# Kernel tuning notes

Measured on AMD Instinct MI355X. Metric: run time of the kernel, lower is better.

## Reference

```python
import jax, jax.numpy as jnp
import numpy as np

B, T, N_OBS, H, N_ACT = 128, 512, 256, 512, 32


def setup_inputs() -> dict:
    key = jax.random.key(0)
    ks = jax.random.split(key, 9)
    s = lambda fan_in: 1.0 / np.sqrt(fan_in)
    return {
        "obs_seq": jax.random.normal(ks[0], (B, T, N_OBS), jnp.float32),
        "h0": jax.random.normal(ks[1], (B, H), jnp.float32),
        "c0": jax.random.normal(ks[2], (B, H), jnp.float32),
        "Wx": jax.random.normal(ks[3], (N_OBS, 4 * H), jnp.float32) * s(N_OBS),
        "Wh": jax.random.normal(ks[4], (H, 4 * H), jnp.float32) * s(H),
        "b": jnp.zeros((4 * H,), jnp.float32),
        "W1": jax.random.normal(ks[5], (H, 512), jnp.float32) * s(H),
        "b1": jnp.zeros((512,), jnp.float32),
        "W2": jax.random.normal(ks[6], (512, 512), jnp.float32) * s(512),
        "b2": jnp.zeros((512,), jnp.float32),
        "Wo": jax.random.normal(ks[7], (512, N_ACT), jnp.float32) * s(512),
        "bo": jnp.zeros((N_ACT,), jnp.float32),
        "action_min": jnp.zeros((N_ACT,), jnp.float32),
        "action_max": jnp.ones((N_ACT,), jnp.float32),
    }


def reference(obs_seq, h0, c0, Wx, Wh, b, W1, b1, W2, b2, Wo, bo, action_min, action_max):
    # Pre-compute input-to-gate projections for all timesteps in one big GEMM,
    # matching flax LSTMCell math: dense_i (no bias) on x, dense_h (bias) on h.
    xg = jnp.einsum('btf,fg->btg', obs_seq, Wx)  # (B, T, 4H)

    def step(carry, xg_t):
        h, c = carry
        z = xg_t + h @ Wh + b  # (B, 4H)
        i, f, g, o = jnp.split(z, 4, axis=-1)
        c = jax.nn.sigmoid(f) * c + jax.nn.sigmoid(i) * jnp.tanh(g)
        h = jax.nn.sigmoid(o) * jnp.tanh(c)
        return (h, c), h

    (h_T, c_T), ys = jax.lax.scan(step, (h0, c0), jnp.swapaxes(xg, 0, 1))
    x = jnp.swapaxes(ys, 0, 1)  # (B, T, H)

    x = jax.nn.relu(x @ W1 + b1)
    x = jax.nn.relu(x @ W2 + b2)
    x = jnp.tanh(x @ Wo + bo)
    action = 0.5 * (x * (action_max - action_min) + (action_max + action_min))
    return action, h_T, c_T
```

## Files before the change

kernel.cpp:

```cpp
#include <hip/hip_runtime.h>

typedef unsigned short u16;
typedef unsigned int u32;
typedef unsigned long long ull;
typedef __attribute__((ext_vector_type(8))) short bf16x8;
typedef __attribute__((ext_vector_type(4))) float f32x4;
typedef __attribute__((ext_vector_type(4))) unsigned u32x4;

#define B_   128
#define T_   512
#define NOBS 256
#define H_   512
#define G4   2048
#define NACT 32
#define M_   (B_*T_)
#define GR   8
#define ROWS 16
#define UN   16
#define ZW   66
#define SENT 0x7FC07FC0u

__device__ __forceinline__ float b2f(u16 s) {
  union { unsigned u; float f; } v; v.u = ((unsigned)s) << 16; return v.f;
}
__device__ __forceinline__ u16 f2b(float f) {
  union { float f; unsigned u; } v; v.f = f;
  unsigned r = v.u + 0x7FFFu + ((v.u >> 16) & 1u);
  return (u16)(r >> 16);
}
__device__ __forceinline__ float sigm(float x) { return 1.f/(1.f+__expf(-x)); }
__device__ __forceinline__ float tanh_f(float x) { return 1.f - 2.f/(1.f+__expf(2.f*x)); }

__device__ __forceinline__ void gld16(const void* g, void* ldsbase) {
#if __has_builtin(__builtin_amdgcn_global_load_lds)
  __builtin_amdgcn_global_load_lds((const __attribute__((address_space(1))) void*)g,
                                   (__attribute__((address_space(3))) void*)ldsbase, 16, 0, 0);
#else
  ((float4*)ldsbase)[threadIdx.x & 63] = *(const float4*)g;
#endif
}

__global__ void k_cvt_obsT(const float* __restrict__ in, u16* __restrict__ out) {
  const long i = (long)blockIdx.x*blockDim.x + threadIdx.x;
  const int k8 = (int)(i & (NOBS/8 - 1));
  const long row = i >> 5;
  const int t = (int)(row >> 7), b = (int)(row & (B_-1));
  const float* src = in + ((long)b*T_ + t)*NOBS + k8*8;
  ushort2 o[4];
  #pragma unroll
  for (int q = 0; q < 4; ++q) {
    o[q].x = f2b(src[q*2]);
    o[q].y = f2b(src[q*2+1]);
  }
  *(ushort2*)&out[i*8+0] = o[0]; *(ushort2*)&out[i*8+2] = o[1];
  *(ushort2*)&out[i*8+4] = o[2]; *(ushort2*)&out[i*8+6] = o[3];
}

__global__ void k_inith(const float* __restrict__ h0, u16* __restrict__ hp) {
  const int i = blockIdx.x*256 + threadIdx.x;
  const int plane = i >> 15, off = i & 32767;
  u32 v;
  if (plane == 0) {
    const int row = off >> 8, p = off & 255;
    v = (unsigned)f2b(h0[row*H_ + 2*p]) | ((unsigned)f2b(h0[row*H_ + 2*p + 1]) << 16);
  } else {
    v = SENT;
  }
  ((u32*)hp)[i] = v;
}

__global__ void k_prep_wT(const float* __restrict__ Wx, const float* __restrict__ Wh,
                          const float* __restrict__ W1, const float* __restrict__ W2,
                          const float* __restrict__ Wo,
                          u16* __restrict__ WxT, u16* __restrict__ WhT,
                          u16* __restrict__ W1T, u16* __restrict__ W2T,
                          u16* __restrict__ WoT) {
  int i = blockIdx.x*256 + threadIdx.x;
  const float* in; u16* out; int R, C;
  if (i < 524288)        { in = Wx; out = WxT; R = NOBS; C = G4; }
  else if (i < 1572864)  { i -= 524288;  in = Wh; out = WhT; R = H_; C = G4; }
  else if (i < 1835008)  { i -= 1572864; in = W1; out = W1T; R = H_; C = H_; }
  else if (i < 2097152)  { i -= 1835008; in = W2; out = W2T; R = H_; C = H_; }
  else                   { i -= 2097152; in = Wo; out = WoT; R = H_; C = NACT; }
  const int c = i / R, r = i - c*R;
  out[i] = f2b(in[r*C + c]);
}

template<int EPI>
__global__ __launch_bounds__(256) void k_gemm_bt(const u16* __restrict__ A, const u16* __restrict__ BT,
                                                 u16* __restrict__ C, const float* __restrict__ bias,
                                                 int M, int N, int K)
{
  __shared__ u16 As[128*64];
  __shared__ u16 Bs[128*64];
  const int tid = threadIdx.x, wv = tid >> 6, lane = tid & 63;
  const int ntile = N >> 7;
  const int tm = blockIdx.x / ntile, tn = blockIdx.x - tm*ntile;
  const int wr = wv >> 1, wc = wv & 1;
  f32x4 acc[4][4];
  for (int m=0;m<4;++m) for (int n=0;n<4;++n) acc[m][n] = (f32x4){0.f,0.f,0.f,0.f};
  const long abase = (long)tm*128, bbase = (long)tn*128;
  const int kit = K >> 6;
  for (int kt = 0; kt < kit; ++kt) {
    const int k0 = kt << 6;
    #pragma unroll
    for (int q = 0; q < 4; ++q) {
      int off = (wv*4+q)*1024 + lane*16;
      int row = off >> 7, colb = off & 127;
      gld16((const char*)A  + ((abase+row)*K + k0)*2 + colb, (char*)As + (wv*4+q)*1024);
      gld16((const char*)BT + ((bbase+row)*K + k0)*2 + colb, (char*)Bs + (wv*4+q)*1024);
    }
    asm volatile("s_waitcnt vmcnt(0)" ::: "memory");
    __syncthreads();
    const int kg = (lane >> 4) * 8;
    #pragma unroll
    for (int kk = 0; kk < 64; kk += 32) {
      bf16x8 af[4], bfr[4];
      #pragma unroll
      for (int m = 0; m < 4; ++m)
        af[m] = *(const bf16x8*)(As + (wr*64 + m*16 + (lane&15))*64 + kk + kg);
      #pragma unroll
      for (int n = 0; n < 4; ++n)
        bfr[n] = *(const bf16x8*)(Bs + (wc*64 + n*16 + (lane&15))*64 + kk + kg);
      #pragma unroll
      for (int m = 0; m < 4; ++m)
        #pragma unroll
        for (int n = 0; n < 4; ++n)
          acc[m][n] = __builtin_amdgcn_mfma_f32_16x16x32_bf16(af[m], bfr[n], acc[m][n], 0, 0, 0);
    }
    __syncthreads();
  }
  const int rq = (lane >> 4) * 4, cl = lane & 15;
  #pragma unroll
  for (int n = 0; n < 4; ++n) {
    const int coln = (int)bbase + wc*64 + n*16 + cl;
    const float bv = (EPI == 1) ? bias[coln] : 0.f;
    #pragma unroll
    for (int m = 0; m < 4; ++m) {
      const long rowb = abase + wr*64 + m*16 + rq;
      #pragma unroll
      for (int q = 0; q < 4; ++q) {
        float v = acc[m][n][q];
        if (EPI == 1) v = fmaxf(v + bv, 0.f);
        C[(rowb+q)*(long)N + coln] = f2b(v);
      }
    }
  }
}

__global__ __launch_bounds__(256, 1) void k_scan(
    const u16* __restrict__ obsT, const u16* __restrict__ WxT, const u16* __restrict__ WhT,
    const float* __restrict__ bvec, const float* __restrict__ c0f,
    u16* __restrict__ hp,
    u16* __restrict__ ys, float* __restrict__ outh, float* __restrict__ outc)
{
  __shared__ u16 Bw[96*64*8];
  __shared__ float zs[2][16*ZW];
  __shared__ float cst[256];
  __shared__ float bsl[64];

  const int tid = threadIdx.x, wv = tid >> 6, lane = tid & 63;
  const int wg = blockIdx.x, isl = wg & (GR-1), cg = wg >> 3;
  const int rb0 = isl*ROWS, S0 = cg*UN;

  const int kh = wv >> 1, ch = wv & 1;
  const int C0 = ch*32;
  const int lq = lane >> 4, l15 = lane & 15;
  const int arow = rb0 + l15;

  for (int idx = tid; idx < 96*64; idx += 256) {
    const int kg = idx >> 6, col = idx & 63;
    const long jrow = (long)((col >> 4)*H_ + S0 + (col & 15));
    const u16* src = (kg < 32) ? (WxT + jrow*NOBS + kg*8)
                               : (WhT + jrow*H_ + (long)(kg-32)*8);
    *(bf16x8*)(Bw + (long)idx*8) = *(const bf16x8*)src;
  }
  cst[tid] = c0f[(rb0 + (tid >> 4))*H_ + S0 + (tid & 15)];
  if (tid < 64) bsl[tid] = bvec[(tid >> 4)*H_ + S0 + (tid & 15)];
  __syncthreads();

  const long fofs = (long)arow*H_ + kh*256 + lq*8;
  const int ldsC = (C0 + l15)*8;

  bf16x8 ax[4];
  {
    const u16* Ax = obsT + (long)arow*NOBS + kh*128 + lq*8;
    #pragma unroll
    for (int ks = 0; ks < 4; ++ks) ax[ks] = *(const bf16x8*)(Ax + ks*32);
  }

  for (int t = 0; t < T_; ++t) {
    f32x4 acc0 = {0.f,0.f,0.f,0.f}, acc1 = {0.f,0.f,0.f,0.f};
    union { u32x4 u; bf16x8 v; } hf[8];
    const u16* haddr = hp + ((long)(t & 7) << 16) + fofs;

    asm volatile("s_waitcnt vmcnt(0)" ::: "memory");

    #pragma unroll
    for (int ks = 0; ks < 8; ++ks)
      asm volatile("global_load_dwordx4 %0, %1, off offset:%2 sc0 sc1"
                   : "=v"(hf[ks].u) : "v"(haddr), "i"(ks*64));

    #pragma unroll
    for (int ks = 0; ks < 4; ++ks) {
      const u16* bp = Bw + (kh*16 + ks*4 + lq)*512 + ldsC;
      bf16x8 b0 = *(const bf16x8*)bp;
      bf16x8 b1 = *(const bf16x8*)(bp + 128);
      acc0 = __builtin_amdgcn_mfma_f32_16x16x32_bf16(ax[ks], b0, acc0, 0, 0, 0);
      acc1 = __builtin_amdgcn_mfma_f32_16x16x32_bf16(ax[ks], b1, acc1, 0, 0, 0);
    }
    __builtin_amdgcn_sched_barrier(0);

    {
      asm volatile("s_waitcnt vmcnt(0)" ::: "memory");
      __builtin_amdgcn_sched_barrier(0);
      unsigned ready = 1u;
      #pragma unroll
      for (int ks = 0; ks < 8; ++ks)
        #pragma unroll
        for (int j = 0; j < 4; ++j)
          ready &= (hf[ks].u[j] != SENT) ? 1u : 0u;
      if (!__all((int)ready)) {
        int spin = 1 << 12;
        for (;;) {
          #pragma unroll
          for (int ks = 0; ks < 8; ++ks)
            asm volatile("global_load_dwordx4 %0, %1, off offset:%2 sc0 sc1"
                         : "=v"(hf[ks].u) : "v"(haddr), "i"(ks*64));
          asm volatile("s_waitcnt vmcnt(0)" ::: "memory");
          __builtin_amdgcn_sched_barrier(0);
          unsigned rdy = 1u;
          #pragma unroll
          for (int ks = 0; ks < 8; ++ks)
            #pragma unroll
            for (int j = 0; j < 4; ++j)
              rdy &= (hf[ks].u[j] != SENT) ? 1u : 0u;
          if (__all((int)rdy)) break;
          if (--spin == 0) break;
        }
      }
    }

    bf16x8 axn[4];
    {
      const int tn = (t+1 < T_) ? t+1 : t;
      const u16* Axn = obsT + ((long)tn*B_ + arow)*NOBS + kh*128 + lq*8;
      #pragma unroll
      for (int ks = 0; ks < 4; ++ks) axn[ks] = *(const bf16x8*)(Axn + ks*32);
    }

    #pragma unroll
    for (int ks = 0; ks < 8; ++ks) {
      const u16* bp = Bw + (32 + kh*32 + ks*4 + lq)*512 + ldsC;
      bf16x8 b0 = *(const bf16x8*)bp;
      bf16x8 b1 = *(const bf16x8*)(bp + 128);
      acc0 = __builtin_amdgcn_mfma_f32_16x16x32_bf16(hf[ks].v, b0, acc0, 0, 0, 0);
      acc1 = __builtin_amdgcn_mfma_f32_16x16x32_bf16(hf[ks].v, b1, acc1, 0, 0, 0);
    }
    #pragma unroll
    for (int ks = 0; ks < 4; ++ks) ax[ks] = axn[ks];

    {
      const int zr0 = lq*4, zc = C0 + l15;
      #pragma unroll
      for (int q = 0; q < 4; ++q) {
        zs[kh][(zr0+q)*ZW + zc]      = acc0[q];
        zs[kh][(zr0+q)*ZW + zc + 16] = acc1[q];
      }
    }
    __syncthreads();

    if (tid < 128) {
      const int rr = tid >> 3, pp = tid & 7;
      float hv2[2], cn2[2];
      #pragma unroll
      for (int u = 0; u < 2; ++u) {
        const int sl = 2*pp + u;
        const float* z0 = &zs[0][rr*ZW];
        const float* z1 = &zs[1][rr*ZW];
        const float zi = z0[sl]    + z1[sl]    + bsl[sl];
        const float zf = z0[16+sl] + z1[16+sl] + bsl[16+sl];
        const float zg = z0[32+sl] + z1[32+sl] + bsl[32+sl];
        const float zo = z0[48+sl] + z1[48+sl] + bsl[48+sl];
        const float cv = cst[rr*16 + sl];
        const float cn = sigm(zf)*cv + sigm(zi)*tanh_f(zg);
        hv2[u] = sigm(zo)*tanh_f(cn);
        cn2[u] = cn;
        cst[rr*16 + sl] = cn;
      }
      const unsigned h01 = (unsigned)f2b(hv2[0]) | ((unsigned)f2b(hv2[1]) << 16);
      const int bq = rb0 + rr;
      const long wofs = (long)bq*H_ + S0 + 2*pp;
      if (t < T_-1)
        __hip_atomic_store((u32*)(hp + ((long)((t+1) & 7) << 16) + wofs), h01,
                           __ATOMIC_RELAXED, __HIP_MEMORY_SCOPE_AGENT);
      __hip_atomic_store((u32*)(hp + ((long)((t+5) & 7) << 16) + wofs), SENT,
                         __ATOMIC_RELAXED, __HIP_MEMORY_SCOPE_AGENT);
      *(u32*)(ys + ((long)bq*T_ + t)*H_ + S0 + 2*pp) = h01;
      if (t == T_-1) {
        outh[bq*H_ + S0 + 2*pp]     = hv2[0];
        outh[bq*H_ + S0 + 2*pp + 1] = hv2[1];
        outc[bq*H_ + S0 + 2*pp]     = cn2[0];
        outc[bq*H_ + S0 + 2*pp + 1] = cn2[1];
      }
    }
  }
}

#define WSW 520
__global__ __launch_bounds__(256) void k_head_mfma(const u16* __restrict__ X,
    const u16* __restrict__ WoT, const float* __restrict__ bo,
    const float* __restrict__ amin, const float* __restrict__ amax,
    float* __restrict__ out)
{
  __shared__ u16 Ws[NACT*WSW];
  const int tid = threadIdx.x, wv = tid >> 6, lane = tid & 63;
  #pragma unroll
  for (int q = 0; q < 8; ++q) {
    const int chunk = q*256 + tid, r = chunk >> 6, c = chunk & 63;
    *(float4*)(Ws + r*WSW + c*8) = ((const float4*)WoT)[chunk];
  }
  __syncthreads();
  const int lq = lane >> 4, l15 = lane & 15;
  const long rb = (long)blockIdx.x*64 + wv*16;
  const u16* Ab = X + (rb + l15)*H_ + lq*8;
  f32x4 acc0 = {0.f,0.f,0.f,0.f}, acc1 = {0.f,0.f,0.f,0.f};
  #pragma unroll
  for (int ks = 0; ks < 16; ++ks) {
    bf16x8 a  = *(const bf16x8*)(Ab + ks*32);
    bf16x8 b0 = *(const bf16x8*)(Ws + l15*WSW + ks*32 + lq*8);
    bf16x8 b1 = *(const bf16x8*)(Ws + (16+l15)*WSW + ks*32 + lq*8);
    acc0 = __builtin_amdgcn_mfma_f32_16x16x32_bf16(a, b0, acc0, 0, 0, 0);
    acc1 = __builtin_amdgcn_mfma_f32_16x16x32_bf16(a, b1, acc1, 0, 0, 0);
  }
  const int c0 = l15, c1 = 16 + l15;
  const float bo0 = bo[c0], bo1 = bo[c1];
  const float a0 = amin[c0], A0 = amax[c0], a1 = amin[c1], A1 = amax[c1];
  #pragma unroll
  for (int q = 0; q < 4; ++q) {
    const long r = rb + lq*4 + q;
    const float y0 = tanh_f(acc0[q] + bo0), y1 = tanh_f(acc1[q] + bo1);
    out[r*NACT + c0] = 0.5f*(y0*(A0 - a0) + (A0 + a0));
    out[r*NACT + c1] = 0.5f*(y1*(A1 - a1) + (A1 + a1));
  }
}

extern "C" void kernel_launch(void* const* d_in, const int* in_sizes, int n_in,
                              void* d_out, int out_size, void* d_ws, size_t ws_size,
                              hipStream_t stream) {
  const float* obs = (const float*)d_in[0];
  const float* h0  = (const float*)d_in[1];
  const float* c0  = (const float*)d_in[2];
  const float* Wx  = (const float*)d_in[3];
  const float* Wh  = (const float*)d_in[4];
  const float* bb  = (const float*)d_in[5];
  const float* W1  = (const float*)d_in[6];
  const float* b1  = (const float*)d_in[7];
  const float* W2  = (const float*)d_in[8];
  const float* b2  = (const float*)d_in[9];
  const float* Wo  = (const float*)d_in[10];
  const float* bo  = (const float*)d_in[11];
  const float* amin= (const float*)d_in[12];
  const float* amax= (const float*)d_in[13];

  char* ws = (char*)d_ws;
  u16* obsT  = (u16*)(ws + 0);
  u16* ys    = (u16*)(ws + 33554432);
  u16* t1    = (u16*)(ws + 100663296);
  u16* t2    = (u16*)(ws + 33554432);
  u16* hp    = (u16*)(ws + 100663296);
  u16* WxT   = (u16*)(ws + 167772160);
  u16* WhT   = (u16*)(ws + 168820736);
  u16* W1T   = (u16*)(ws + 170917888);
  u16* W2T   = (u16*)(ws + 171442176);
  u16* WoT   = (u16*)(ws + 171966464);

  float* outA = (float*)d_out;
  float* outh = outA + (long)M_*NACT;
  float* outc = outh + B_*H_;

  k_cvt_obsT<<<M_*NOBS/8/256, 256, 0, stream>>>(obs, obsT);
  k_inith<<<1024, 256, 0, stream>>>(h0, hp);
  k_prep_wT<<<8256, 256, 0, stream>>>(Wx, Wh, W1, W2, Wo, WxT, WhT, W1T, W2T, WoT);

  k_scan<<<256, 256, 0, stream>>>(obsT, WxT, WhT, bb, c0, hp, ys, outh, outc);

  k_gemm_bt<1><<<(M_/128)*(H_/128), 256, 0, stream>>>(ys, W1T, t1, b1, M_, H_, H_);
  k_gemm_bt<1><<<(M_/128)*(H_/128), 256, 0, stream>>>(t1, W2T, t2, b2, M_, H_, H_);
  k_head_mfma<<<M_/64, 256, 0, stream>>>(t2, WoT, bo, amin, amax, outA);
}
```

Measured before the change: 1.473 ms.

## Keep scan weights in registers and pack two column slices per block

The persistent LSTM scan kernel now holds each wave's Wx and Wh weight fragments in VGPRs for all timesteps instead of reading them from LDS every step. It also merges two column-slice workgroups into one 512-thread block, so the grid is 128 blocks of 512 threads instead of 256 of 256, with per-slice shared buffers for gate partial sums, cell state and bias. This removes per-step LDS weight traffic from the serial recurrence. The cost is much higher register pressure (24 bf16x8 weight vectors per lane) with possible spills, and a block-wide barrier that now couples two slices.

After: 2.756 ms. +87.0%, slower.

```diff
diff --git a/kernel.cpp b/kernel.cpp
--- a/kernel.cpp
+++ b/kernel.cpp
@@ -148,39 +148,52 @@
   }
 }
 
-__global__ __launch_bounds__(256, 1) void k_scan(
+__global__ __launch_bounds__(512, 1) void k_scan(
     const u16* __restrict__ obsT, const u16* __restrict__ WxT, const u16* __restrict__ WhT,
     const float* __restrict__ bvec, const float* __restrict__ c0f,
     u16* __restrict__ hp,
     u16* __restrict__ ys, float* __restrict__ outh, float* __restrict__ outc)
 {
-  __shared__ u16 Bw[96*64*8];
-  __shared__ float zs[2][16*ZW];
-  __shared__ float cst[256];
-  __shared__ float bsl[64];
-
-  const int tid = threadIdx.x, wv = tid >> 6, lane = tid & 63;
-  const int wg = blockIdx.x, isl = wg & (GR-1), cg = wg >> 3;
+  __shared__ float zs[2][2][16*ZW];
+  __shared__ float cst[2][256];
+  __shared__ float bsl[2][64];
+
+  const int tid = threadIdx.x;
+  const int slice = tid >> 8;
+  const int ltid = tid & 255;
+  const int wv4 = (tid >> 6) & 3;
+  const int lane = tid & 63;
+  const int wg = blockIdx.x, isl = wg & (GR-1), sgrp = wg >> 3;
+  const int cg = sgrp*2 + slice;
   const int rb0 = isl*ROWS, S0 = cg*UN;
 
-  const int kh = wv >> 1, ch = wv & 1;
+  const int kh = wv4 >> 1, ch = wv4 & 1;
   const int C0 = ch*32;
   const int lq = lane >> 4, l15 = lane & 15;
   const int arow = rb0 + l15;
 
-  for (int idx = tid; idx < 96*64; idx += 256) {
-    const int kg = idx >> 6, col = idx & 63;
-    const long jrow = (long)((col >> 4)*H_ + S0 + (col & 15));
-    const u16* src = (kg < 32) ? (WxT + jrow*NOBS + kg*8)
-                               : (WhT + jrow*H_ + (long)(kg-32)*8);
-    *(bf16x8*)(Bw + (long)idx*8) = *(const bf16x8*)src;
-  }
-  cst[tid] = c0f[(rb0 + (tid >> 4))*H_ + S0 + (tid & 15)];
-  if (tid < 64) bsl[tid] = bvec[(tid >> 4)*H_ + S0 + (tid & 15)];
+  const int j0 = C0 + l15, j1 = j0 + 16;
+  const long w0 = (long)((j0 >> 4)*H_ + S0 + (j0 & 15));
+  const long w1 = (long)((j1 >> 4)*H_ + S0 + (j1 & 15));
+  bf16x8 wbx[4][2], wbh[8][2];
+  #pragma unroll
+  for (int ks = 0; ks < 4; ++ks) {
+    const long k = (long)kh*128 + ks*32 + lq*8;
+    wbx[ks][0] = *(const bf16x8*)(WxT + w0*NOBS + k);
+    wbx[ks][1] = *(const bf16x8*)(WxT + w1*NOBS + k);
+  }
+  #pragma unroll
+  for (int ks = 0; ks < 8; ++ks) {
+    const long k = (long)kh*256 + ks*32 + lq*8;
+    wbh[ks][0] = *(const bf16x8*)(WhT + w0*H_ + k);
+    wbh[ks][1] = *(const bf16x8*)(WhT + w1*H_ + k);
+  }
+
+  cst[slice][ltid] = c0f[(rb0 + (ltid >> 4))*H_ + S0 + (ltid & 15)];
+  if (ltid < 64) bsl[slice][ltid] = bvec[(ltid >> 4)*H_ + S0 + (ltid & 15)];
   __syncthreads();
 
   const long fofs = (long)arow*H_ + kh*256 + lq*8;
-  const int ldsC = (C0 + l15)*8;
 
   bf16x8 ax[4];
   {
@@ -203,11 +216,8 @@
 
     #pragma unroll
     for (int ks = 0; ks < 4; ++ks) {
-      const u16* bp = Bw + (kh*16 + ks*4 + lq)*512 + ldsC;
-      bf16x8 b0 = *(const bf16x8*)bp;
-      bf16x8 b1 = *(const bf16x8*)(bp + 128);
-      acc0 = __builtin_amdgcn_mfma_f32_16x16x32_bf16(ax[ks], b0, acc0, 0, 0, 0);
-      acc1 = __builtin_amdgcn_mfma_f32_16x16x32_bf16(ax[ks], b1, acc1, 0, 0, 0);
+      acc0 = __builtin_amdgcn_mfma_f32_16x16x32_bf16(ax[ks], wbx[ks][0], acc0, 0, 0, 0);
+      acc1 = __builtin_amdgcn_mfma_f32_16x16x32_bf16(ax[ks], wbx[ks][1], acc1, 0, 0, 0);
     }
     __builtin_amdgcn_sched_barrier(0);
 
@@ -251,11 +261,8 @@
 
     #pragma unroll
     for (int ks = 0; ks < 8; ++ks) {
-      const u16* bp = Bw + (32 + kh*32 + ks*4 + lq)*512 + ldsC;
-      bf16x8 b0 = *(const bf16x8*)bp;
-      bf16x8 b1 = *(const bf16x8*)(bp + 128);
-      acc0 = __builtin_amdgcn_mfma_f32_16x16x32_bf16(hf[ks].v, b0, acc0, 0, 0, 0);
-      acc1 = __builtin_amdgcn_mfma_f32_16x16x32_bf16(hf[ks].v, b1, acc1, 0, 0, 0);
+      acc0 = __builtin_amdgcn_mfma_f32_16x16x32_bf16(hf[ks].v, wbh[ks][0], acc0, 0, 0, 0);
+      acc1 = __builtin_amdgcn_mfma_f32_16x16x32_bf16(hf[ks].v, wbh[ks][1], acc1, 0, 0, 0);
     }
     #pragma unroll
     for (int ks = 0; ks < 4; ++ks) ax[ks] = axn[ks];
@@ -264,29 +271,29 @@
       const int zr0 = lq*4, zc = C0 + l15;
       #pragma unroll
       for (int q = 0; q < 4; ++q) {
-        zs[kh][(zr0+q)*ZW + zc]      = acc0[q];
-        zs[kh][(zr0+q)*ZW + zc + 16] = acc1[q];
+        zs[slice][kh][(zr0+q)*ZW + zc]      = acc0[q];
+        zs[slice][kh][(zr0+q)*ZW + zc + 16] = acc1[q];
       }
     }
     __syncthreads();
 
-    if (tid < 128) {
-      const int rr = tid >> 3, pp = tid & 7;
+    if (ltid < 128) {
+      const int rr = ltid >> 3, pp = ltid & 7;
       float hv2[2], cn2[2];
       #pragma unroll
       for (int u = 0; u < 2; ++u) {
         const int sl = 2*pp + u;
-        const float* z0 = &zs[0][rr*ZW];
-        const float* z1 = &zs[1][rr*ZW];
-        const float zi = z0[sl]    + z1[sl]    + bsl[sl];
-        const float zf = z0[16+sl] + z1[16+sl] + bsl[16+sl];
-        const float zg = z0[32+sl] + z1[32+sl] + bsl[32+sl];
-        const float zo = z0[48+sl] + z1[48+sl] + bsl[48+sl];
-        const float cv = cst[rr*16 + sl];
+        const float* z0 = &zs[slice][0][rr*ZW];
+        const float* z1 = &zs[slice][1][rr*ZW];
+        const float zi = z0[sl]    + z1[sl]    + bsl[slice][sl];
+        const float zf = z0[16+sl] + z1[16+sl] + bsl[slice][16+sl];
+        const float zg = z0[32+sl] + z1[32+sl] + bsl[slice][32+sl];
+        const float zo = z0[48+sl] + z1[48+sl] + bsl[slice][48+sl];
+        const float cv = cst[slice][rr*16 + sl];
         const float cn = sigm(zf)*cv + sigm(zi)*tanh_f(zg);
         hv2[u] = sigm(zo)*tanh_f(cn);
         cn2[u] = cn;
-        cst[rr*16 + sl] = cn;
+        cst[slice][rr*16 + sl] = cn;
       }
       const unsigned h01 = (unsigned)f2b(hv2[0]) | ((unsigned)f2b(hv2[1]) << 16);
       const int bq = rb0 + rr;
@@ -383,7 +390,7 @@
   k_inith<<<1024, 256, 0, stream>>>(h0, hp);
   k_prep_wT<<<8256, 256, 0, stream>>>(Wx, Wh, W1, W2, Wo, WxT, WhT, W1T, W2T, WoT);
 
-  k_scan<<<256, 256, 0, stream>>>(obsT, WxT, WhT, bb, c0, hp, ys, outh, outc);
+  k_scan<<<128, 512, 0, stream>>>(obsT, WxT, WhT, bb, c0, hp, ys, outh, outc);
 
   k_gemm_bt<1><<<(M_/128)*(H_/128), 256, 0, stream>>>(ys, W1T, t1, b1, M_, H_, H_);
   k_gemm_bt<1><<<(M_/128)*(H_/128), 256, 0, stream>>>(t1, W2T, t2, b2, M_, H_, H_);
```

## Interleave four batch sub-groups per workgroup in the LSTM scan

Applied to the files above, without the earlier changes.

Each scan workgroup now owns four interleaved 4-row batch sub-groups instead of one contiguous 16-row slab. Each timestep processes the sub-groups in turn: it loads h, spin-waits for readiness, runs the MFMA, applies the gates, and publishes the new h. The intent is that while one sub-group waits on other workgroups' h, another sub-group's data is likely already ready, which hides the cross-workgroup synchronisation latency. The cost is more serial rounds and barriers per step. The MFMA also computes 16 rows where only 4 are distinct, and only 32 threads do the gate math.

After: 4.077 ms. 177% more time.

```diff
diff --git a/kernel.cpp b/kernel.cpp
--- a/kernel.cpp
+++ b/kernel.cpp
@@ -14,8 +14,7 @@
 #define G4   2048
 #define NACT 32
 #define M_   (B_*T_)
-#define GR   8
-#define ROWS 16
+#define NS   4
 #define UN   16
 #define ZW   66
 #define SENT 0x7FC07FC0u
@@ -155,18 +154,18 @@
     u16* __restrict__ ys, float* __restrict__ outh, float* __restrict__ outc)
 {
   __shared__ u16 Bw[96*64*8];
-  __shared__ float zs[2][16*ZW];
-  __shared__ float cst[256];
+  __shared__ float zs[2][2][16*ZW];
+  __shared__ float cst[NS][64];
   __shared__ float bsl[64];
 
   const int tid = threadIdx.x, wv = tid >> 6, lane = tid & 63;
-  const int wg = blockIdx.x, isl = wg & (GR-1), cg = wg >> 3;
-  const int rb0 = isl*ROWS, S0 = cg*UN;
+  const int wg = blockIdx.x, g = wg & 7, cg = wg >> 3;
+  const int S0 = cg*UN;
 
   const int kh = wv >> 1, ch = wv & 1;
   const int C0 = ch*32;
   const int lq = lane >> 4, l15 = lane & 15;
-  const int arow = rb0 + l15;
+  const int r4 = l15 & 3;
 
   for (int idx = tid; idx < 96*64; idx += 256) {
     const int kg = idx >> 6, col = idx & 63;
@@ -175,133 +174,141 @@
                                : (WhT + jrow*H_ + (long)(kg-32)*8);
     *(bf16x8*)(Bw + (long)idx*8) = *(const bf16x8*)src;
   }
-  cst[tid] = c0f[(rb0 + (tid >> 4))*H_ + S0 + (tid & 15)];
-  if (tid < 64) bsl[tid] = bvec[(tid >> 4)*H_ + S0 + (tid & 15)];
+  if (tid < 64) {
+    bsl[tid] = bvec[(tid >> 4)*H_ + S0 + (tid & 15)];
+    #pragma unroll
+    for (int s = 0; s < NS; ++s)
+      cst[s][tid] = c0f[(4*g + 32*s + (tid >> 4))*H_ + S0 + (tid & 15)];
+  }
   __syncthreads();
 
-  const long fofs = (long)arow*H_ + kh*256 + lq*8;
   const int ldsC = (C0 + l15)*8;
 
-  bf16x8 ax[4];
-  {
+  bf16x8 ax[NS][4];
+  #pragma unroll
+  for (int s = 0; s < NS; ++s) {
+    const int arow = 4*g + 32*s + r4;
     const u16* Ax = obsT + (long)arow*NOBS + kh*128 + lq*8;
     #pragma unroll
-    for (int ks = 0; ks < 4; ++ks) ax[ks] = *(const bf16x8*)(Ax + ks*32);
+    for (int ks = 0; ks < 4; ++ks) ax[s][ks] = *(const bf16x8*)(Ax + ks*32);
   }
 
   for (int t = 0; t < T_; ++t) {
-    f32x4 acc0 = {0.f,0.f,0.f,0.f}, acc1 = {0.f,0.f,0.f,0.f};
-    union { u32x4 u; bf16x8 v; } hf[8];
-    const u16* haddr = hp + ((long)(t & 7) << 16) + fofs;
-
-    asm volatile("s_waitcnt vmcnt(0)" ::: "memory");
-
-    #pragma unroll
-    for (int ks = 0; ks < 8; ++ks)
-      asm volatile("global_load_dwordx4 %0, %1, off offset:%2 sc0 sc1"
-                   : "=v"(hf[ks].u) : "v"(haddr), "i"(ks*64));
-
-    #pragma unroll
-    for (int ks = 0; ks < 4; ++ks) {
-      const u16* bp = Bw + (kh*16 + ks*4 + lq)*512 + ldsC;
-      bf16x8 b0 = *(const bf16x8*)bp;
-      bf16x8 b1 = *(const bf16x8*)(bp + 128);
-      acc0 = __builtin_amdgcn_mfma_f32_16x16x32_bf16(ax[ks], b0, acc0, 0, 0, 0);
-      acc1 = __builtin_amdgcn_mfma_f32_16x16x32_bf16(ax[ks], b1, acc1, 0, 0, 0);
-    }
-    __builtin_amdgcn_sched_barrier(0);
-
-    {
+    #pragma unroll
+    for (int s = 0; s < NS; ++s) {
+      const int rb0 = 4*g + 32*s;
+      const int arow = rb0 + r4;
+      const long fofs = (long)arow*H_ + kh*256 + lq*8;
+      const u16* haddr = hp + ((long)(t & 7) << 16) + fofs;
+
       asm volatile("s_waitcnt vmcnt(0)" ::: "memory");
+
+      union { u32x4 u; bf16x8 v; } hf[8];
+      #pragma unroll
+      for (int ks = 0; ks < 8; ++ks)
+        asm volatile("global_load_dwordx4 %0, %1, off offset:%2 sc0 sc1"
+                     : "=v"(hf[ks].u) : "v"(haddr), "i"(ks*64));
+
+      f32x4 acc0 = {0.f,0.f,0.f,0.f}, acc1 = {0.f,0.f,0.f,0.f};
+      #pragma unroll
+      for (int ks = 0; ks < 4; ++ks) {
+        const u16* bp = Bw + (kh*16 + ks*4 + lq)*512 + ldsC;
+        bf16x8 b0 = *(const bf16x8*)bp;
+        bf16x8 b1 = *(const bf16x8*)(bp + 128);
+        acc0 = __builtin_amdgcn_mfma_f32_16x16x32_bf16(ax[s][ks], b0, acc0, 0, 0, 0);
+        acc1 = __builtin_amdgcn_mfma_f32_16x16x32_bf16(ax[s][ks], b1, acc1, 0, 0, 0);
+      }
       __builtin_amdgcn_sched_barrier(0);
-      unsigned ready = 1u;
-      #pragma unroll
-      for (int ks = 0; ks < 8; ++ks)
-        #pragma unroll
-        for (int j = 0; j < 4; ++j)
-          ready &= (hf[ks].u[j] != SENT) ? 1u : 0u;
-      if (!__all((int)ready)) {
-        int spin = 1 << 12;
-        for (;;) {
+
+      {
+        asm volatile("s_waitcnt vmcnt(0)" ::: "memory");
+        __builtin_amdgcn_sched_barrier(0);
+        unsigned ready = 1u;
+        #pragma unroll
+        for (int ks = 0; ks < 8; ++ks)
           #pragma unroll
-          for (int ks = 0; ks < 8; ++ks)
-            asm volatile("global_load_dwordx4 %0, %1, off offset:%2 sc0 sc1"
-                         : "=v"(hf[ks].u) : "v"(haddr), "i"(ks*64));
-          asm volatile("s_waitcnt vmcnt(0)" ::: "memory");
-          __builtin_amdgcn_sched_barrier(0);
-          unsigned rdy = 1u;
-          #pragma unroll
-          for (int ks = 0; ks < 8; ++ks)
+          for (int j = 0; j < 4; ++j)
+            ready &= (hf[ks].u[j] != SENT) ? 1u : 0u;
+        if (!__all((int)ready)) {
+          int spin = 1 << 12;
+          for (;;) {
             #pragma unroll
-            for (int j = 0; j < 4; ++j)
-              rdy &= (hf[ks].u[j] != SENT) ? 1u : 0u;
-          if (__all((int)rdy)) break;
-          if (--spin == 0) break;
+            for (int ks = 0; ks < 8; ++ks)
+              asm volatile("global_load_dwordx4 %0, %1, off offset:%2 sc0 sc1"
+                           : "=v"(hf[ks].u) : "v"(haddr), "i"(ks*64));
+            asm volatile("s_waitcnt vmcnt(0)" ::: "memory");
+            __builtin_amdgcn_sched_barrier(0);
+            unsigned rdy = 1u;
+            #pragma unroll
+            for (int ks = 0; ks < 8; ++ks)
+              #pragma unroll
+              for (int j = 0; j < 4; ++j)
+                rdy &= (hf[ks].u[j] != SENT) ? 1u : 0u;
+            if (__all((int)rdy)) break;
+            if (--spin == 0) break;
+          }
         }
       }
-    }
-
-    bf16x8 axn[4];
-    {
-      const int tn = (t+1 < T_) ? t+1 : t;
-      const u16* Axn = obsT + ((long)tn*B_ + arow)*NOBS + kh*128 + lq*8;
-      #pragma unroll
-      for (int ks = 0; ks < 4; ++ks) axn[ks] = *(const bf16x8*)(Axn + ks*32);
-    }
-
-    #pragma unroll
-    for (int ks = 0; ks < 8; ++ks) {
-      const u16* bp = Bw + (32 + kh*32 + ks*4 + lq)*512 + ldsC;
-      bf16x8 b0 = *(const bf16x8*)bp;
-      bf16x8 b1 = *(const bf16x8*)(bp + 128);
-      acc0 = __builtin_amdgcn_mfma_f32_16x16x32_bf16(hf[ks].v, b0, acc0, 0, 0, 0);
-      acc1 = __builtin_amdgcn_mfma_f32_16x16x32_bf16(hf[ks].v, b1, acc1, 0, 0, 0);
-    }
-    #pragma unroll
-    for (int ks = 0; ks < 4; ++ks) ax[ks] = axn[ks];
-
-    {
-      const int zr0 = lq*4, zc = C0 + l15;
-      #pragma unroll
-      for (int q = 0; q < 4; ++q) {
-        zs[kh][(zr0+q)*ZW + zc]      = acc0[q];
-        zs[kh][(zr0+q)*ZW + zc + 16] = acc1[q];
-      }
-    }
-    __syncthreads();
-
-    if (tid < 128) {
-      const int rr = tid >> 3, pp = tid & 7;
-      float hv2[2], cn2[2];
-      #pragma unroll
-      for (int u = 0; u < 2; ++u) {
-        const int sl = 2*pp + u;
-        const float* z0 = &zs[0][rr*ZW];
-        const float* z1 = &zs[1][rr*ZW];
-        const float zi = z0[sl]    + z1[sl]    + bsl[sl];
-        const float zf = z0[16+sl] + z1[16+sl] + bsl[16+sl];
-        const float zg = z0[32+sl] + z1[32+sl] + bsl[32+sl];
-        const float zo = z0[48+sl] + z1[48+sl] + bsl[48+sl];
-        const float cv = cst[rr*16 + sl];
-        const float cn = sigm(zf)*cv + sigm(zi)*tanh_f(zg);
-        hv2[u] = sigm(zo)*tanh_f(cn);
-        cn2[u] = cn;
-        cst[rr*16 + sl] = cn;
-      }
-      const unsigned h01 = (unsigned)f2b(hv2[0]) | ((unsigned)f2b(hv2[1]) << 16);
-      const int bq = rb0 + rr;
-      const long wofs = (long)bq*H_ + S0 + 2*pp;
-      if (t < T_-1)
-        __hip_atomic_store((u32*)(hp + ((long)((t+1) & 7) << 16) + wofs), h01,
+
+      {
+        const int tn = (t+1 < T_) ? t+1 : t;
+        const u16* Axn = obsT + ((long)tn*B_ + arow)*NOBS + kh*128 + lq*8;
+        #pragma unroll
+        for (int ks = 0; ks < 4; ++ks) ax[s][ks] = *(const bf16x8*)(Axn + ks*32);
+      }
+
+      #pragma unroll
+      for (int ks = 0; ks < 8; ++ks) {
+        const u16* bp = Bw + (32 + kh*32 + ks*4 + lq)*512 + ldsC;
+        bf16x8 b0 = *(const bf16x8*)bp;
+        bf16x8 b1 = *(const bf16x8*)(bp + 128);
+        acc0 = __builtin_amdgcn_mfma_f32_16x16x32_bf16(hf[ks].v, b0, acc0, 0, 0, 0);
+        acc1 = __builtin_amdgcn_mfma_f32_16x16x32_bf16(hf[ks].v, b1, acc1, 0, 0, 0);
+      }
+
+      {
+        const int zr0 = lq*4, zc = C0 + l15;
+        #pragma unroll
+        for (int q = 0; q < 4; ++q) {
+          zs[s & 1][kh][(zr0+q)*ZW + zc]      = acc0[q];
+          zs[s & 1][kh][(zr0+q)*ZW + zc + 16] = acc1[q];
+        }
+      }
+      __syncthreads();
+
+      if (tid < 32) {
+        const int rr = tid >> 3, pp = tid & 7;
+        float hv2[2], cn2[2];
+        #pragma unroll
+        for (int u = 0; u < 2; ++u) {
+          const int sl = 2*pp + u;
+          const float* z0 = &zs[s & 1][0][rr*ZW];
+          const float* z1 = &zs[s & 1][1][rr*ZW];
+          const float zi = z0[sl]    + z1[sl]    + bsl[sl];
+          const float zf = z0[16+sl] + z1[16+sl] + bsl[16+sl];
+          const float zg = z0[32+sl] + z1[32+sl] + bsl[32+sl];
+          const float zo = z0[48+sl] + z1[48+sl] + bsl[48+sl];
+          const float cv = cst[s][rr*16 + sl];
+          const float cn = sigm(zf)*cv + sigm(zi)*tanh_f(zg);
+          hv2[u] = sigm(zo)*tanh_f(cn);
+          cn2[u] = cn;
+          cst[s][rr*16 + sl] = cn;
+        }
+        const unsigned h01 = (unsigned)f2b(hv2[0]) | ((unsigned)f2b(hv2[1]) << 16);
+        const int bq = rb0 + rr;
+        const long wofs = (long)bq*H_ + S0 + 2*pp;
+        if (t < T_-1)
+          __hip_atomic_store((u32*)(hp + ((long)((t+1) & 7) << 16) + wofs), h01,
+                             __ATOMIC_RELAXED, __HIP_MEMORY_SCOPE_AGENT);
+        __hip_atomic_store((u32*)(hp + ((long)((t+5) & 7) << 16) + wofs), SENT,
                            __ATOMIC_RELAXED, __HIP_MEMORY_SCOPE_AGENT);
-      __hip_atomic_store((u32*)(hp + ((long)((t+5) & 7) << 16) + wofs), SENT,
-                         __ATOMIC_RELAXED, __HIP_MEMORY_SCOPE_AGENT);
-      *(u32*)(ys + ((long)bq*T_ + t)*H_ + S0 + 2*pp) = h01;
-      if (t == T_-1) {
-        outh[bq*H_ + S0 + 2*pp]     = hv2[0];
-        outh[bq*H_ + S0 + 2*pp + 1] = hv2[1];
-        outc[bq*H_ + S0 + 2*pp]     = cn2[0];
-        outc[bq*H_ + S0 + 2*pp + 1] = cn2[1];
+        *(u32*)(ys + ((long)bq*T_ + t)*H_ + S0 + 2*pp) = h01;
+        if (t == T_-1) {
+          outh[bq*H_ + S0 + 2*pp]     = hv2[0];
+          outh[bq*H_ + S0 + 2*pp + 1] = hv2[1];
+          outc[bq*H_ + S0 + 2*pp]     = cn2[0];
+          outc[bq*H_ + S0 + 2*pp + 1] = cn2[1];
+        }
       }
     }
   }
```
